# Kernel tuning notes

Hardware: AMD Instinct MI355X
Metric: run time of the kernel (lower is better)

The kernel has to match this reference:

```python
import jax, jax.numpy as jnp
import numpy as np
import math

B, C = 512, 100000
H_PARAM = 0.333
S_PARAM = 64.0
M_PARAM = 0.4
T_ALPHA = 1.0
EPS = 1e-06


def setup_inputs() -> dict:
    key = jax.random.key(0)
    k1, k2, k3 = jax.random.split(key, 3)
    # cosine similarities in (-1, 1)
    logits = jax.random.uniform(k1, (B, C), dtype=jnp.float32, minval=-1.0, maxval=1.0)
    # embedding L2 norms: positive, roughly in a realistic range ~[5, 45]
    norms = jax.random.uniform(k2, (B, 1), dtype=jnp.float32, minval=5.0, maxval=45.0)
    labels = jax.random.randint(k3, (B,), 0, C, dtype=jnp.int64)
    return {"logits": logits, "norms": norms, "labels": labels}


def reference(logits, norms, labels):
    # t_alpha = 1.0 in training mode => batch_mean/std buffers equal the
    # current batch statistics exactly (torch.std is unbiased, ddof=1).
    cosine = jnp.clip(logits, -1.0 + EPS, 1.0 - EPS)              # [B, C]
    safe_norms = jax.lax.stop_gradient(jnp.clip(norms, 0.001, 100.0))  # [B, 1]

    mean = jnp.mean(safe_norms)
    std = jnp.std(safe_norms, ddof=1)

    margin_scaler = (safe_norms - mean) / (std + EPS) * H_PARAM   # [B, 1]
    margin_scaler = jnp.clip(margin_scaler, -1.0, 1.0)

    onehot = jax.nn.one_hot(labels, C, dtype=cosine.dtype)        # [B, C]

    g_angular = -M_PARAM * margin_scaler                          # [B, 1]
    theta = jnp.arccos(cosine)                                    # [B, C]
    theta_m = jnp.clip(theta + onehot * g_angular, EPS, math.pi - EPS)

    g_add = M_PARAM + M_PARAM * margin_scaler                     # [B, 1]
    cosine_m_final = jnp.cos(theta_m) - onehot * g_add            # [B, C]
    scaled = cosine_m_final * S_PARAM

    # mean cross-entropy over the batch
    logp = jax.nn.log_softmax(scaled, axis=-1)                    # [B, C]
    nll = -jnp.take_along_axis(logp, labels[:, None], axis=1)[:, 0]
    return jnp.mean(nll)
```

## Files before the change

### kernel.cpp

```cpp
#include <hip/hip_runtime.h>
#include <math.h>

#define B_SZ 512
#define C_SZ 100000
#define H_PARAM 0.333f
#define S_PARAM 64.0f
#define M_PARAM 0.4f
#define EPS 1e-6f
#define PI_F 3.14159265358979323846f

__device__ inline float waveReduceSum(float v) {
#pragma unroll
    for (int off = 32; off > 0; off >>= 1) v += __shfl_xor(v, off, 64);
    return v;
}

__global__ __launch_bounds__(512) void stats_kernel(
    const float* __restrict__ norms,
    float* __restrict__ g_ang,
    float* __restrict__ g_add) {
    __shared__ float sh[8];
    int i = threadIdx.x;
    float n = fminf(fmaxf(norms[i], 0.001f), 100.0f);

    int wave = i >> 6, lane = i & 63;
    float wsum = waveReduceSum(n);
    if (lane == 0) sh[wave] = wsum;
    __syncthreads();
    float total = 0.f;
#pragma unroll
    for (int w = 0; w < 8; ++w) total += sh[w];
    float mean = total * (1.0f / 512.0f);
    __syncthreads();

    float d = n - mean;
    float wss = waveReduceSum(d * d);
    if (lane == 0) sh[wave] = wss;
    __syncthreads();
    float tss = 0.f;
#pragma unroll
    for (int w = 0; w < 8; ++w) tss += sh[w];
    float sd = sqrtf(tss / 511.0f);

    float ms = (n - mean) / (sd + EPS) * H_PARAM;
    ms = fminf(fmaxf(ms, -1.0f), 1.0f);
    g_ang[i] = -M_PARAM * ms;
    g_add[i] = M_PARAM + M_PARAM * ms;
}

__global__ __launch_bounds__(256) void row_kernel(
    const float* __restrict__ logits,
    const int* __restrict__ labels,
    const float* __restrict__ g_ang,
    const float* __restrict__ g_add,
    float* __restrict__ nll) {
    int row = blockIdx.x;
    int label = labels[row];
    const float* lr = logits + (size_t)row * C_SZ;

    __shared__ float s_target;
    __shared__ float shl[4];
    if (threadIdx.x == 0) {
        float c = lr[label];
        c = fminf(fmaxf(c, -1.0f + EPS), 1.0f - EPS);
        float theta = acosf(c);
        float tm = theta + g_ang[row];
        tm = fminf(fmaxf(tm, EPS), PI_F - EPS);
        s_target = (cosf(tm) - g_add[row]) * S_PARAM;
    }
    __syncthreads();
    float target = s_target;

    float l = 0.f;
    const float4* lr4 = (const float4*)lr;
    const int nchunk = C_SZ / 4;
    for (int j4 = threadIdx.x; j4 < nchunk; j4 += 256) {
        float4 v = lr4[j4];
        int jbase = j4 * 4;
        float vals[4] = {v.x, v.y, v.z, v.w};
#pragma unroll
        for (int k = 0; k < 4; ++k) {
            float c = fminf(fmaxf(vals[k], -1.0f + EPS), 1.0f - EPS);
            float sc = S_PARAM * c - S_PARAM;
            if (jbase + k == label) sc = target - S_PARAM;
            l += __expf(sc);
        }
    }

    float lsum = waveReduceSum(l);
    int wave = threadIdx.x >> 6, lane = threadIdx.x & 63;
    if (lane == 0) shl[wave] = lsum;
    __syncthreads();
    if (threadIdx.x == 0) {
        float t = shl[0] + shl[1] + shl[2] + shl[3];
        nll[row] = S_PARAM + logf(t) - target;
    }
}

__global__ __launch_bounds__(512) void mean_kernel(
    const float* __restrict__ nll,
    float* __restrict__ out) {
    __shared__ float sh[8];
    int i = threadIdx.x;
    float v = nll[i];
    int wave = i >> 6, lane = i & 63;
    float wsum = waveReduceSum(v);
    if (lane == 0) sh[wave] = wsum;
    __syncthreads();
    if (i == 0) {
        float total = 0.f;
#pragma unroll
        for (int w = 0; w < 8; ++w) total += sh[w];
        out[0] = total * (1.0f / 512.0f);
    }
}

extern "C" void kernel_launch(void* const* d_in, const int* in_sizes, int n_in,
                              void* d_out, int out_size, void* d_ws, size_t ws_size,
                              hipStream_t stream) {
    const float* logits = (const float*)d_in[0];
    const float* norms  = (const float*)d_in[1];
    const int*   labels = (const int*)d_in[2];
    float* out = (float*)d_out;

    float* g_ang = (float*)d_ws;
    float* g_add = g_ang + B_SZ;
    float* nll   = g_add + B_SZ;

    stats_kernel<<<1, 512, 0, stream>>>(norms, g_ang, g_add);
    row_kernel<<<B_SZ, 256, 0, stream>>>(logits, labels, g_ang, g_add, nll);
    mean_kernel<<<1, 512, 0, stream>>>(nll, out);
}
```

Measured before the change: 299.7 us.

## Split each row across four blocks and correct label term afterwards

The row kernel now launches four blocks per row, each summing exponentials over a quarter of the columns and atomically adding into a per-row accumulator. The per-row target logit is computed up front in the stats kernel. The label column is no longer special-cased in the hot loop; its plain exp term is subtracted and the margin-adjusted one added in the final kernel. This is meant to raise parallelism from 512 blocks and drop the per-element label compare, at the cost of atomics and a possible cancellation error in the subtraction.

```diff
diff --git a/kernel.cpp b/kernel.cpp
--- a/kernel.cpp
+++ b/kernel.cpp
@@ -9,16 +9,27 @@
 #define EPS 1e-6f
 #define PI_F 3.14159265358979323846f
 
+#define CHUNKS_PER_ROW 4
+#define F4_PER_ROW (C_SZ / 4)
+#define F4_PER_CHUNK (F4_PER_ROW / CHUNKS_PER_ROW)
+
 __device__ inline float waveReduceSum(float v) {
 #pragma unroll
     for (int off = 32; off > 0; off >>= 1) v += __shfl_xor(v, off, 64);
     return v;
 }
 
+__device__ inline float clip1(float x) {
+    return fminf(fmaxf(x, -1.0f + EPS), 1.0f - EPS);
+}
+
 __global__ __launch_bounds__(512) void stats_kernel(
     const float* __restrict__ norms,
-    float* __restrict__ g_ang,
-    float* __restrict__ g_add) {
+    const float* __restrict__ logits,
+    const int* __restrict__ labels,
+    float* __restrict__ target,
+    float* __restrict__ plain,
+    float* __restrict__ acc) {
     __shared__ float sh[8];
     int i = threadIdx.x;
     float n = fminf(fmaxf(norms[i], 0.001f), 100.0f);
@@ -44,65 +55,59 @@
 
     float ms = (n - mean) / (sd + EPS) * H_PARAM;
     ms = fminf(fmaxf(ms, -1.0f), 1.0f);
-    g_ang[i] = -M_PARAM * ms;
-    g_add[i] = M_PARAM + M_PARAM * ms;
+    float g_ang = -M_PARAM * ms;
+    float g_add = M_PARAM + M_PARAM * ms;
+
+    int lab = labels[i];
+    float c = clip1(logits[(size_t)i * C_SZ + lab]);
+    float theta = acosf(c);
+    float tm = fminf(fmaxf(theta + g_ang, EPS), PI_F - EPS);
+    float t = (cosf(tm) - g_add) * S_PARAM;
+
+    target[i] = t;
+    plain[i] = __expf(S_PARAM * c - S_PARAM);
+    acc[i] = 0.f;
 }
 
 __global__ __launch_bounds__(256) void row_kernel(
     const float* __restrict__ logits,
-    const int* __restrict__ labels,
-    const float* __restrict__ g_ang,
-    const float* __restrict__ g_add,
-    float* __restrict__ nll) {
-    int row = blockIdx.x;
-    int label = labels[row];
-    const float* lr = logits + (size_t)row * C_SZ;
-
-    __shared__ float s_target;
-    __shared__ float shl[4];
-    if (threadIdx.x == 0) {
-        float c = lr[label];
-        c = fminf(fmaxf(c, -1.0f + EPS), 1.0f - EPS);
-        float theta = acosf(c);
-        float tm = theta + g_ang[row];
-        tm = fminf(fmaxf(tm, EPS), PI_F - EPS);
-        s_target = (cosf(tm) - g_add[row]) * S_PARAM;
-    }
-    __syncthreads();
-    float target = s_target;
+    float* __restrict__ acc) {
+    int row = blockIdx.x >> 2;
+    int chunk = blockIdx.x & 3;
+    const float4* lr4 = (const float4*)(logits + (size_t)row * C_SZ);
+    int begin = chunk * F4_PER_CHUNK;
+    int end = begin + F4_PER_CHUNK;
 
     float l = 0.f;
-    const float4* lr4 = (const float4*)lr;
-    const int nchunk = C_SZ / 4;
-    for (int j4 = threadIdx.x; j4 < nchunk; j4 += 256) {
-        float4 v = lr4[j4];
-        int jbase = j4 * 4;
-        float vals[4] = {v.x, v.y, v.z, v.w};
-#pragma unroll
-        for (int k = 0; k < 4; ++k) {
-            float c = fminf(fmaxf(vals[k], -1.0f + EPS), 1.0f - EPS);
-            float sc = S_PARAM * c - S_PARAM;
-            if (jbase + k == label) sc = target - S_PARAM;
-            l += __expf(sc);
-        }
+    for (int j = begin + threadIdx.x; j < end; j += 256) {
+        float4 v = lr4[j];
+        l += __expf(fmaf(S_PARAM, clip1(v.x), -S_PARAM));
+        l += __expf(fmaf(S_PARAM, clip1(v.y), -S_PARAM));
+        l += __expf(fmaf(S_PARAM, clip1(v.z), -S_PARAM));
+        l += __expf(fmaf(S_PARAM, clip1(v.w), -S_PARAM));
     }
 
-    float lsum = waveReduceSum(l);
+    __shared__ float shl[4];
     int wave = threadIdx.x >> 6, lane = threadIdx.x & 63;
-    if (lane == 0) shl[wave] = lsum;
+    float wsum = waveReduceSum(l);
+    if (lane == 0) shl[wave] = wsum;
     __syncthreads();
     if (threadIdx.x == 0) {
-        float t = shl[0] + shl[1] + shl[2] + shl[3];
-        nll[row] = S_PARAM + logf(t) - target;
+        atomicAdd(&acc[row], shl[0] + shl[1] + shl[2] + shl[3]);
     }
 }
 
-__global__ __launch_bounds__(512) void mean_kernel(
-    const float* __restrict__ nll,
+__global__ __launch_bounds__(512) void final_kernel(
+    const float* __restrict__ acc,
+    const float* __restrict__ target,
+    const float* __restrict__ plain,
     float* __restrict__ out) {
     __shared__ float sh[8];
     int i = threadIdx.x;
-    float v = nll[i];
+    float t = target[i];
+    float s = acc[i] - plain[i] + __expf(t - S_PARAM);
+    float v = S_PARAM + logf(s) - t;
+
     int wave = i >> 6, lane = i & 63;
     float wsum = waveReduceSum(v);
     if (lane == 0) sh[wave] = wsum;
@@ -123,11 +128,11 @@
     const int*   labels = (const int*)d_in[2];
     float* out = (float*)d_out;
 
-    float* g_ang = (float*)d_ws;
-    float* g_add = g_ang + B_SZ;
-    float* nll   = g_add + B_SZ;
+    float* target = (float*)d_ws;
+    float* plain  = target + B_SZ;
+    float* acc    = plain + B_SZ;
 
-    stats_kernel<<<1, 512, 0, stream>>>(norms, g_ang, g_add);
-    row_kernel<<<B_SZ, 256, 0, stream>>>(logits, labels, g_ang, g_add, nll);
-    mean_kernel<<<1, 512, 0, stream>>>(nll, out);
+    stats_kernel<<<1, 512, 0, stream>>>(norms, logits, labels, target, plain, acc);
+    row_kernel<<<B_SZ * CHUNKS_PER_ROW, 256, 0, stream>>>(logits, acc);
+    final_kernel<<<1, 512, 0, stream>>>(acc, target, plain, out);
 }
```

Measured after the change: 289.5 us. 1.04x faster.
